# Kernel optimization log

Measured on AMD Instinct MI355X. Metric: run time of the kernel, lower is better.

Reference implementation:

```python
import jax, jax.numpy as jnp
import numpy as np

I, L, T, S = 128, 8, 128, 128   # input neurons, topo batches, neurons per batch, fan-in span
BIG = 1e9
EPS = 1e-5


def setup_inputs() -> dict:
    key = jax.random.key(0)
    ks = jax.random.split(key, 7)
    x = jax.random.normal(ks[0], (I,), jnp.float32)
    # per-neuron weights|bias, scaled down for numerical stability of softmax/gelu chain
    W = jax.random.normal(ks[1], (L, T, S + 1), jnp.float32) * 0.05
    mask = (jax.random.uniform(ks[2], (L, T, S)) > 0.5).astype(jnp.float32)  # DAG connectivity
    attn_t = jax.random.normal(ks[3], (L, 3, S, S + 1), jnp.float32) * 0.05      # topo q/k/v (weight|bias)
    attn_n = jax.random.normal(ks[4], (L, T, 3, S, S + 1), jnp.float32) * 0.05   # per-neuron q/k/v
    # additive attention mask: attend only over a neuron's actual inputs
    attn_mask_n = BIG * (1.0 - mask[:, :, :, None] * mask[:, :, None, :])        # (L,T,S,S)
    norm_params = jnp.stack([jnp.ones((L, S)), jnp.zeros((L, S))], 1) \
        + 0.1 * jax.random.normal(ks[5], (L, 2, S), jnp.float32)                 # gamma, beta
    ada = jnp.ones((L, T, 2), jnp.float32) \
        + 0.1 * jax.random.normal(ks[6], (L, T, 2), jnp.float32)                 # gain, amplification
    span_ids = jnp.arange(L * S, dtype=jnp.int32).reshape(L, S)    # gather indices per topo batch
    tb_ids = I + jnp.arange(L * T, dtype=jnp.int32).reshape(L, T)  # scatter indices per topo batch
    return dict(x=x, W=W, mask=mask, attn_t=attn_t, attn_n=attn_n,
                attn_mask_n=attn_mask_n, norm_params=norm_params, ada=ada,
                span_ids=span_ids, tb_ids=tb_ids)


def _attention(qkv, vals, amask):
    # qkv: (3, S, S+1) stacked query/key/value (weight|bias); vals: (S,)
    wq, bq = qkv[0, :, :-1], qkv[0, :, -1]
    wk, bk = qkv[1, :, :-1], qkv[1, :, -1]
    wv, bv = qkv[2, :, :-1], qkv[2, :, -1]
    q = wq @ vals + bq
    k = wk @ vals + bk
    v = wv @ vals + bv
    scores = jnp.outer(q, k) * jax.lax.rsqrt(jnp.float32(vals.shape[0])) - amask
    return jax.nn.softmax(scores) @ v + vals  # residual connection


def _forward(x, W, mask, attn_t, attn_n, attn_mask_n, norm_params, ada, span_ids, tb_ids):
    values = jnp.zeros((I + L * T,), x.dtype).at[jnp.arange(I)].set(x)
    for b in range(L):  # fixed, small topological batch order
        vals = values[span_ids[b]]                                  # gather fan-in span (S,)
        mu = jnp.mean(vals)
        var = jnp.var(vals)
        vals = (vals - mu) * jax.lax.rsqrt(var + EPS)               # topo norm (standardize)
        vals = vals * norm_params[b, 0] + norm_params[b, 1]
        vals = _attention(attn_t[b], vals, 0.0)                     # topo-level self-attention
        # neuron-level self-attention, vmapped over the batch's T neurons -> (T, S)
        vals_n = jax.vmap(_attention, in_axes=(0, None, 0))(attn_n[b], vals, attn_mask_n[b])
        w, bias = W[b, :, :-1], W[b, :, -1]
        aff = jnp.einsum('ts,ts->t', w * mask[b], vals_n) + bias    # masked affine per neuron
        if b == L - 1:
            out = aff                                               # output neurons: identity transform
        else:
            out = jax.nn.gelu(aff * ada[b, :, 0]) * ada[b, :, 1]    # adaptive activation a*sigma(b*x)
        values = values.at[tb_ids[b]].set(out)
    return values[tb_ids[L - 1]]


def reference(x, W, mask, attn_t, attn_n, attn_mask_n, norm_params, ada, span_ids, tb_ids):
    return _forward(x, W, mask, attn_t, attn_n, attn_mask_n, norm_params, ada, span_ids, tb_ids)
```

## Files before the change

### kernel.cpp

```cpp
#include <hip/hip_runtime.h>
#include <math.h>

#define L_DIM 8
#define T_DIM 128
#define S_DIM 128
#define SP1   129
#define BIGF  1000000000.0f
#define EPSF  1e-5f
#define NTHREADS 1024
#define NWAVES 16

template<int CTRL>
__device__ __forceinline__ float dpp_add_part(float x) {
    int r = __builtin_amdgcn_update_dpp(0, __float_as_int(x), CTRL, 0xF, 0xF, false);
    return __int_as_float(r);
}
template<int CTRL>
__device__ __forceinline__ float dpp_self(float x) {
    int r = __builtin_amdgcn_update_dpp(__float_as_int(x), __float_as_int(x), CTRL, 0xF, 0xF, false);
    return __int_as_float(r);
}
__device__ __forceinline__ float dppSum63(float x) {
    x += dpp_add_part<0x111>(x);
    x += dpp_add_part<0x112>(x);
    x += dpp_add_part<0x114>(x);
    x += dpp_add_part<0x118>(x);
    x += dpp_add_part<0x142>(x);
    x += dpp_add_part<0x143>(x);
    return x;
}
__device__ __forceinline__ float dppMax63(float x) {
    x = fmaxf(x, dpp_self<0x111>(x));
    x = fmaxf(x, dpp_self<0x112>(x));
    x = fmaxf(x, dpp_self<0x114>(x));
    x = fmaxf(x, dpp_self<0x118>(x));
    x = fmaxf(x, dpp_self<0x142>(x));
    x = fmaxf(x, dpp_self<0x143>(x));
    return x;
}
__device__ __forceinline__ float lane63(float x) {
    return __int_as_float(__builtin_amdgcn_readlane(__float_as_int(x), 63));
}

__device__ __forceinline__ void qkv_matvec(const float* __restrict__ base,
                                           float vin0, float vin1,
                                           int lane, int wid,
                                           float* __restrict__ lds_q,
                                           float* __restrict__ lds_k,
                                           float* __restrict__ lds_v)
{
#pragma unroll
    for (int it = 0; it < 3; ++it) {
        float* dst = (it == 0) ? lds_q : (it == 1) ? lds_k : lds_v;
        const float* bb = base + (size_t)it * S_DIM * SP1;
        float lo[8], hi[8], bias[8], acc[8];
#pragma unroll
        for (int u = 0; u < 8; ++u) {
            const float* row = bb + (size_t)(wid + u * NWAVES) * SP1;
            lo[u]   = row[lane];
            hi[u]   = row[lane + 64];
            bias[u] = row[128];
        }
#pragma unroll
        for (int u = 0; u < 8; ++u) acc[u] = lo[u] * vin0 + hi[u] * vin1;
#pragma unroll
        for (int u = 0; u < 8; ++u) acc[u] = dppSum63(acc[u]);
        if (lane == 63) {
#pragma unroll
            for (int u = 0; u < 8; ++u) dst[wid + u * NWAVES] = acc[u] + bias[u];
        }
    }
}

template <bool MASKED>
__device__ __forceinline__ void attn_softmax(int lane, int wid,
                                             const float* __restrict__ lds_q,
                                             const float* __restrict__ lds_k,
                                             const float* __restrict__ lds_v,
                                             const float* __restrict__ lds_m,
                                             const float* __restrict__ resid,
                                             float* __restrict__ lds_out)
{
    const float scale = 0.08838834764831845f;
    float k0 = lds_k[lane], k1 = lds_k[lane + 64];
    float v0 = lds_v[lane], v1 = lds_v[lane + 64];
    float m0 = 0.0f, m1 = 0.0f;
    if (MASKED) { m0 = lds_m[lane]; m1 = lds_m[lane + 64]; }

    float s1[8], s2[8], mx[8];
#pragma unroll
    for (int u = 0; u < 8; ++u) {
        int r = wid + u * NWAVES;
        float q = lds_q[r];
        float a1v = 0.0f, a2v = 0.0f;
        if (MASKED) {
            float mr = lds_m[r];
            a1v = BIGF * (1.0f - mr * m0);
            a2v = BIGF * (1.0f - mr * m1);
        }
        s1[u] = q * k0 * scale - a1v;
        s2[u] = q * k1 * scale - a2v;
    }
#pragma unroll
    for (int u = 0; u < 8; ++u) mx[u] = lane63(dppMax63(fmaxf(s1[u], s2[u])));
    float den[8], num[8];
#pragma unroll
    for (int u = 0; u < 8; ++u) {
        float e1 = __expf(s1[u] - mx[u]);
        float e2 = __expf(s2[u] - mx[u]);
        den[u] = e1 + e2;
        num[u] = e1 * v0 + e2 * v1;
    }
#pragma unroll
    for (int u = 0; u < 8; ++u) { den[u] = dppSum63(den[u]); num[u] = dppSum63(num[u]); }
    if (lane == 63) {
#pragma unroll
        for (int u = 0; u < 8; ++u) {
            int r = wid + u * NWAVES;
            lds_out[r] = num[u] / den[u] + resid[r];
        }
    }
}

__global__ __launch_bounds__(NTHREADS)
void net_kernel(const float* __restrict__ x,
                const float* __restrict__ W,
                const float* __restrict__ maskp,
                const float* __restrict__ attn_t,
                const float* __restrict__ attn_n,
                const float* __restrict__ norm_params,
                const float* __restrict__ ada,
                float* __restrict__ out,
                unsigned long long* __restrict__ mbox)
{
    const int t    = blockIdx.x;
    const int tid  = threadIdx.x;
    const int lane = tid & 63;
    const int wid  = tid >> 6;

    __shared__ float lds_vals[S_DIM];
    __shared__ float lds_q[S_DIM], lds_k[S_DIM], lds_v[S_DIM];
    __shared__ float lds_tv[S_DIM];
    __shared__ float lds_vn[S_DIM];
    __shared__ float lds_m[S_DIM];
    __shared__ float lds_red[NWAVES];

    for (int b = 0; b < L_DIM; ++b) {
        if (tid < S_DIM) {
            float v;
            if (b == 0) {
                v = x[tid];
            } else {
                const unsigned long long* mb = mbox + (size_t)(b - 1) * T_DIM;
                unsigned long long w;
                do {
                    w = __hip_atomic_load(&mb[tid], __ATOMIC_RELAXED, __HIP_MEMORY_SCOPE_AGENT);
                } while ((unsigned int)(w >> 32) != (unsigned int)b);
                float raw = __uint_as_float((unsigned int)w);
                float a0 = ada[((b - 1) * T_DIM + tid) * 2 + 0];
                float a1 = ada[((b - 1) * T_DIM + tid) * 2 + 1];
                float z  = raw * a0;
                float z3 = z * z * z;
                float g  = 0.5f * z * (1.0f + tanhf(0.7978845608028654f * (z + 0.044715f * z3)));
                v = g * a1;
            }
            lds_vals[tid] = v;
            lds_m[tid] = maskp[(b * T_DIM + t) * S_DIM + tid];
        }
        __syncthreads();

        {
            float v = (tid < S_DIM) ? lds_vals[tid] : 0.0f;
            float s = lane63(dppSum63(v));
            if (lane == 0) lds_red[wid] = s;
            __syncthreads();
            float tot = 0.0f;
            for (int i = 0; i < NWAVES; ++i) tot += lds_red[i];
            float mu = tot * (1.0f / 128.0f);
            __syncthreads();
            float d = (tid < S_DIM) ? (v - mu) : 0.0f;
            float s2 = lane63(dppSum63(d * d));
            if (lane == 0) lds_red[wid] = s2;
            __syncthreads();
            float tot2 = 0.0f;
            for (int i = 0; i < NWAVES; ++i) tot2 += lds_red[i];
            float var = tot2 * (1.0f / 128.0f);
            float rstd = rsqrtf(var + EPSF);
            if (tid < S_DIM) {
                float np0 = norm_params[(b * 2 + 0) * S_DIM + tid];
                float np1 = norm_params[(b * 2 + 1) * S_DIM + tid];
                lds_vals[tid] = (v - mu) * rstd * np0 + np1;
            }
            __syncthreads();
        }

        {
            float vin0 = lds_vals[lane], vin1 = lds_vals[lane + 64];
            qkv_matvec(attn_t + (size_t)b * 3 * S_DIM * SP1, vin0, vin1,
                       lane, wid, lds_q, lds_k, lds_v);
        }
        __syncthreads();

        attn_softmax<false>(lane, wid, lds_q, lds_k, lds_v, lds_m, lds_vals, lds_tv);
        __syncthreads();

        {
            float tv0 = lds_tv[lane], tv1 = lds_tv[lane + 64];
            qkv_matvec(attn_n + (size_t)(b * T_DIM + t) * 3 * S_DIM * SP1, tv0, tv1,
                       lane, wid, lds_q, lds_k, lds_v);
        }
        __syncthreads();

        attn_softmax<true>(lane, wid, lds_q, lds_k, lds_v, lds_m, lds_tv, lds_vn);
        __syncthreads();

        {
            const float* wrow = W + (size_t)(b * T_DIM + t) * SP1;
            float term = (tid < S_DIM) ? wrow[tid] * lds_m[tid] * lds_vn[tid] : 0.0f;
            float s = dppSum63(term);
            if (lane == 63) lds_red[wid] = s;
            __syncthreads();
            if (tid == 0) {
                float aff = wrow[128];
                for (int i = 0; i < NWAVES; ++i) aff += lds_red[i];
                if (b == L_DIM - 1) {
                    out[t] = aff;
                } else {
                    unsigned long long w =
                        ((unsigned long long)(unsigned int)(b + 1) << 32) |
                        (unsigned long long)__float_as_uint(aff);
                    __hip_atomic_store(&mbox[(size_t)b * T_DIM + t], w,
                                       __ATOMIC_RELAXED, __HIP_MEMORY_SCOPE_AGENT);
                }
            }
        }
        __syncthreads();
    }
}

extern "C" void kernel_launch(void* const* d_in, const int* in_sizes, int n_in,
                              void* d_out, int out_size, void* d_ws, size_t ws_size,
                              hipStream_t stream) {
    const float* x           = (const float*)d_in[0];
    const float* W           = (const float*)d_in[1];
    const float* maskp       = (const float*)d_in[2];
    const float* attn_t      = (const float*)d_in[3];
    const float* attn_n      = (const float*)d_in[4];
    const float* norm_params = (const float*)d_in[6];
    const float* ada         = (const float*)d_in[7];
    float* out = (float*)d_out;

    unsigned long long* mbox = (unsigned long long*)d_ws;

    hipMemsetAsync(d_ws, 0, (size_t)(L_DIM - 1) * T_DIM * sizeof(unsigned long long), stream);

    void* args[] = { (void*)&x, (void*)&W, (void*)&maskp, (void*)&attn_t, (void*)&attn_n,
                     (void*)&norm_params, (void*)&ada, (void*)&out, (void*)&mbox };
    hipLaunchCooperativeKernel((const void*)net_kernel, dim3(T_DIM), dim3(NTHREADS),
                               args, 0, stream);
}
```

Before: 492.9 us.

## Split each neuron's attention across two blocks with cross-block K/V exchange

Doubles the grid so that two blocks share each neuron. Each block computes half of the per-neuron q/k/v rows and half of the masked softmax rows. The blocks swap their K/V halves and the partial affine sums through tagged global mailboxes. This spreads the dominant per-neuron attn_n weight streaming over twice as many CUs. The cost is extra spin-wait synchronisation between the paired blocks, and each block still redundantly computes the topo-level attention.

```diff
diff --git a/kernel.cpp b/kernel.cpp
--- a/kernel.cpp
+++ b/kernel.cpp
@@ -72,34 +72,23 @@
     }
 }
 
-template <bool MASKED>
-__device__ __forceinline__ void attn_softmax(int lane, int wid,
-                                             const float* __restrict__ lds_q,
-                                             const float* __restrict__ lds_k,
-                                             const float* __restrict__ lds_v,
-                                             const float* __restrict__ lds_m,
-                                             const float* __restrict__ resid,
-                                             float* __restrict__ lds_out)
+__device__ __forceinline__ void attn_softmax_full(int lane, int wid,
+                                                  const float* __restrict__ lds_q,
+                                                  const float* __restrict__ lds_k,
+                                                  const float* __restrict__ lds_v,
+                                                  const float* __restrict__ resid,
+                                                  float* __restrict__ lds_out)
 {
     const float scale = 0.08838834764831845f;
     float k0 = lds_k[lane], k1 = lds_k[lane + 64];
     float v0 = lds_v[lane], v1 = lds_v[lane + 64];
-    float m0 = 0.0f, m1 = 0.0f;
-    if (MASKED) { m0 = lds_m[lane]; m1 = lds_m[lane + 64]; }
 
     float s1[8], s2[8], mx[8];
 #pragma unroll
     for (int u = 0; u < 8; ++u) {
-        int r = wid + u * NWAVES;
-        float q = lds_q[r];
-        float a1v = 0.0f, a2v = 0.0f;
-        if (MASKED) {
-            float mr = lds_m[r];
-            a1v = BIGF * (1.0f - mr * m0);
-            a2v = BIGF * (1.0f - mr * m1);
-        }
-        s1[u] = q * k0 * scale - a1v;
-        s2[u] = q * k1 * scale - a2v;
+        float q = lds_q[wid + u * NWAVES];
+        s1[u] = q * k0 * scale;
+        s2[u] = q * k1 * scale;
     }
 #pragma unroll
     for (int u = 0; u < 8; ++u) mx[u] = lane63(dppMax63(fmaxf(s1[u], s2[u])));
@@ -131,9 +120,13 @@
                 const float* __restrict__ norm_params,
                 const float* __restrict__ ada,
                 float* __restrict__ out,
-                unsigned long long* __restrict__ mbox)
+                unsigned long long* __restrict__ mbox,
+                unsigned long long* __restrict__ kvx,
+                unsigned long long* __restrict__ paff)
 {
-    const int t    = blockIdx.x;
+    const int bx   = blockIdx.x;
+    const int t    = bx & (T_DIM - 1);
+    const int h    = bx >> 7;
     const int tid  = threadIdx.x;
     const int lane = tid & 63;
     const int wid  = tid >> 6;
@@ -144,6 +137,8 @@
     __shared__ float lds_vn[S_DIM];
     __shared__ float lds_m[S_DIM];
     __shared__ float lds_red[NWAVES];
+
+    const float scale = 0.08838834764831845f;
 
     for (int b = 0; b < L_DIM; ++b) {
         if (tid < S_DIM) {
@@ -201,36 +196,126 @@
         }
         __syncthreads();
 
-        attn_softmax<false>(lane, wid, lds_q, lds_k, lds_v, lds_m, lds_vals, lds_tv);
+        attn_softmax_full(lane, wid, lds_q, lds_k, lds_v, lds_vals, lds_tv);
         __syncthreads();
 
         {
+            const float* base = attn_n + (size_t)(b * T_DIM + t) * 3 * S_DIM * SP1;
             float tv0 = lds_tv[lane], tv1 = lds_tv[lane + 64];
-            qkv_matvec(attn_n + (size_t)(b * T_DIM + t) * 3 * S_DIM * SP1, tv0, tv1,
-                       lane, wid, lds_q, lds_k, lds_v);
-        }
-        __syncthreads();
-
-        attn_softmax<true>(lane, wid, lds_q, lds_k, lds_v, lds_m, lds_tv, lds_vn);
+            float lo[12], hi[12], bias[12], acc[12];
+#pragma unroll
+            for (int c = 0; c < 3; ++c) {
+#pragma unroll
+                for (int u = 0; u < 4; ++u) {
+                    int i = c * 4 + u;
+                    int r = h * 64 + (wid << 2) + u;
+                    const float* row = base + ((size_t)c * S_DIM + r) * SP1;
+                    lo[i]   = row[lane];
+                    hi[i]   = row[lane + 64];
+                    bias[i] = row[128];
+                }
+            }
+#pragma unroll
+            for (int i = 0; i < 12; ++i) acc[i] = lo[i] * tv0 + hi[i] * tv1;
+#pragma unroll
+            for (int i = 0; i < 12; ++i) acc[i] = dppSum63(acc[i]);
+            if (lane == 63) {
+                unsigned long long* myslots = kvx + ((size_t)t * 2 + h) * 128;
+                unsigned long long tag = (unsigned long long)(unsigned int)(b + 1) << 32;
+#pragma unroll
+                for (int c = 0; c < 3; ++c) {
+#pragma unroll
+                    for (int u = 0; u < 4; ++u) {
+                        int i = c * 4 + u;
+                        int j = (wid << 2) + u;
+                        int r = h * 64 + j;
+                        float val = acc[i] + bias[i];
+                        if (c == 0) {
+                            lds_q[r] = val;
+                        } else if (c == 1) {
+                            lds_k[r] = val;
+                            __hip_atomic_store(&myslots[j], tag | __float_as_uint(val),
+                                               __ATOMIC_RELAXED, __HIP_MEMORY_SCOPE_AGENT);
+                        } else {
+                            lds_v[r] = val;
+                            __hip_atomic_store(&myslots[64 + j], tag | __float_as_uint(val),
+                                               __ATOMIC_RELAXED, __HIP_MEMORY_SCOPE_AGENT);
+                        }
+                    }
+                }
+            }
+        }
+
+        if (tid < 128) {
+            const unsigned long long* slot = kvx + ((size_t)t * 2 + (1 - h)) * 128 + tid;
+            unsigned long long w;
+            do {
+                w = __hip_atomic_load(slot, __ATOMIC_RELAXED, __HIP_MEMORY_SCOPE_AGENT);
+            } while ((unsigned int)(w >> 32) != (unsigned int)(b + 1));
+            float val = __uint_as_float((unsigned int)w);
+            int r = (1 - h) * 64 + (tid & 63);
+            if (tid < 64) lds_k[r] = val; else lds_v[r] = val;
+        }
         __syncthreads();
 
         {
+            float k0 = lds_k[lane], k1 = lds_k[lane + 64];
+            float v0 = lds_v[lane], v1 = lds_v[lane + 64];
+            float m0 = lds_m[lane], m1 = lds_m[lane + 64];
+            float s1[4], s2[4], mx[4];
+#pragma unroll
+            for (int u = 0; u < 4; ++u) {
+                int r = h * 64 + (wid << 2) + u;
+                float q  = lds_q[r];
+                float mr = lds_m[r];
+                s1[u] = q * k0 * scale - BIGF * (1.0f - mr * m0);
+                s2[u] = q * k1 * scale - BIGF * (1.0f - mr * m1);
+            }
+#pragma unroll
+            for (int u = 0; u < 4; ++u) mx[u] = lane63(dppMax63(fmaxf(s1[u], s2[u])));
+            float den[4], num[4];
+#pragma unroll
+            for (int u = 0; u < 4; ++u) {
+                float e1 = __expf(s1[u] - mx[u]);
+                float e2 = __expf(s2[u] - mx[u]);
+                den[u] = e1 + e2;
+                num[u] = e1 * v0 + e2 * v1;
+            }
+#pragma unroll
+            for (int u = 0; u < 4; ++u) { den[u] = dppSum63(den[u]); num[u] = dppSum63(num[u]); }
+            if (lane == 63) {
+#pragma unroll
+                for (int u = 0; u < 4; ++u) {
+                    int r = h * 64 + (wid << 2) + u;
+                    lds_vn[r] = num[u] / den[u] + lds_tv[r];
+                }
+            }
+        }
+        __syncthreads();
+
+        if (tid < 64) {
             const float* wrow = W + (size_t)(b * T_DIM + t) * SP1;
-            float term = (tid < S_DIM) ? wrow[tid] * lds_m[tid] * lds_vn[tid] : 0.0f;
-            float s = dppSum63(term);
-            if (lane == 63) lds_red[wid] = s;
-            __syncthreads();
-            if (tid == 0) {
-                float aff = wrow[128];
-                for (int i = 0; i < NWAVES; ++i) aff += lds_red[i];
-                if (b == L_DIM - 1) {
-                    out[t] = aff;
+            int s = h * 64 + lane;
+            float term = wrow[s] * lds_m[s] * lds_vn[s];
+            float p = dppSum63(term);
+            if (lane == 63) {
+                unsigned long long tag = (unsigned long long)(unsigned int)(b + 1) << 32;
+                if (h == 1) {
+                    __hip_atomic_store(&paff[t], tag | __float_as_uint(p),
+                                       __ATOMIC_RELAXED, __HIP_MEMORY_SCOPE_AGENT);
                 } else {
-                    unsigned long long w =
-                        ((unsigned long long)(unsigned int)(b + 1) << 32) |
-                        (unsigned long long)__float_as_uint(aff);
-                    __hip_atomic_store(&mbox[(size_t)b * T_DIM + t], w,
-                                       __ATOMIC_RELAXED, __HIP_MEMORY_SCOPE_AGENT);
+                    unsigned long long w;
+                    do {
+                        w = __hip_atomic_load(&paff[t], __ATOMIC_RELAXED, __HIP_MEMORY_SCOPE_AGENT);
+                    } while ((unsigned int)(w >> 32) != (unsigned int)(b + 1));
+                    float aff = p + __uint_as_float((unsigned int)w) + wrow[128];
+                    if (b == L_DIM - 1) {
+                        out[t] = aff;
+                    } else {
+                        __hip_atomic_store(&mbox[(size_t)b * T_DIM + t],
+                                           tag | __float_as_uint(aff),
+                                           __ATOMIC_RELAXED, __HIP_MEMORY_SCOPE_AGENT);
+                    }
                 }
             }
         }
@@ -251,11 +336,14 @@
     float* out = (float*)d_out;
 
     unsigned long long* mbox = (unsigned long long*)d_ws;
-
-    hipMemsetAsync(d_ws, 0, (size_t)(L_DIM - 1) * T_DIM * sizeof(unsigned long long), stream);
+    unsigned long long* kvx  = (unsigned long long*)((char*)d_ws + 7168);
+    unsigned long long* paff = (unsigned long long*)((char*)d_ws + 7168 + 262144);
+
+    hipMemsetAsync(d_ws, 0, 7168 + 262144 + 1024, stream);
 
     void* args[] = { (void*)&x, (void*)&W, (void*)&maskp, (void*)&attn_t, (void*)&attn_n,
-                     (void*)&norm_params, (void*)&ada, (void*)&out, (void*)&mbox };
-    hipLaunchCooperativeKernel((const void*)net_kernel, dim3(T_DIM), dim3(NTHREADS),
+                     (void*)&norm_params, (void*)&ada, (void*)&out,
+                     (void*)&mbox, (void*)&kvx, (void*)&paff };
+    hipLaunchCooperativeKernel((const void*)net_kernel, dim3(2 * T_DIM), dim3(NTHREADS),
                                args, 0, stream);
 }
```

Result: no change. 501.4 us (+1.7%).
